# Kernel optimization log

Measured on AMD Instinct MI355X. Metric: run time of the kernel, lower is better.

The kernel has to match this reference:

```python
import jax, jax.numpy as jnp
import numpy as np

D_MODEL = 1024
N_HEADS = 16
HEAD_DIM = D_MODEL // N_HEADS


def setup_inputs() -> dict:
    key = jax.random.key(0)
    k_x, k_w1, k_b1, k_w2, k_b2 = jax.random.split(key, 5)
    B, S = 4, 2048
    x = jax.random.normal(k_x, (B, S, D_MODEL), dtype=jnp.float32)
    # torch Linear init ~ U(-1/sqrt(fan_in), 1/sqrt(fan_in))
    lim = 1.0 / np.sqrt(D_MODEL)
    qkv_w = jax.random.uniform(k_w1, (D_MODEL, 3 * D_MODEL), jnp.float32, -lim, lim)
    qkv_b = jax.random.uniform(k_b1, (3 * D_MODEL,), jnp.float32, -lim, lim)
    out_w = jax.random.uniform(k_w2, (D_MODEL, D_MODEL), jnp.float32, -lim, lim)
    out_b = jax.random.uniform(k_b2, (D_MODEL,), jnp.float32, -lim, lim)
    return {"x": x, "qkv_w": qkv_w, "qkv_b": qkv_b, "out_w": out_w, "out_b": out_b}


def reference(x, qkv_w, qkv_b, out_w, out_b):
    B, S, D = x.shape
    scale = HEAD_DIM ** -0.5
    qkv = x @ qkv_w + qkv_b  # [B,S,3D]
    q, k, v = jnp.split(qkv, 3, axis=-1)
    def to_heads(t):
        return t.reshape(B, S, N_HEADS, HEAD_DIM).transpose(0, 2, 1, 3)  # [B,H,S,Dh]
    q, k, v = to_heads(q), to_heads(k), to_heads(v)
    scores = jnp.einsum('bhqd,bhkd->bhqk', q, k) * scale  # [B,H,S,S]
    causal = jnp.tril(jnp.ones((S, S), dtype=bool))
    scores = jnp.where(causal, scores, -jnp.inf)
    weights = jax.nn.softmax(scores, axis=-1)  # dropout is identity in eval
    out = jnp.einsum('bhqk,bhkd->bhqd', weights, v)  # [B,H,S,Dh]
    out = out.transpose(0, 2, 1, 3).reshape(B, S, D)
    return out @ out_w + out_b
```

## Files before the change

kernel.cpp:

```cpp
#include <hip/hip_runtime.h>

typedef __bf16 bf16x8 __attribute__((ext_vector_type(8)));
typedef float f32x4 __attribute__((ext_vector_type(4)));
typedef unsigned short u16;

#define D_MODEL 1024
#define SEQ     2048
#define BATCH   4
#define NH      16
#define DH      64

#define QSCALE 0.18033688011f

#define SWZ(b) ((b) ^ ((((b) >> 8) & 3) << 5) ^ ((((b) >> 7) & 1) << 4))

static __device__ __forceinline__ u16 f2bf(float f) {
    union { float f; unsigned u; } v; v.f = f;
    unsigned r = v.u + 0x7FFF + ((v.u >> 16) & 1);
    return (u16)(r >> 16);
}
static __device__ __forceinline__ void storeC(u16* C, size_t off, float v) { C[off] = f2bf(v); }
static __device__ __forceinline__ void storeC(float* C, size_t off, float v) { C[off] = v; }

static __device__ __forceinline__ void async_ld16(u16* lds, const u16* g) {
    __builtin_amdgcn_global_load_lds(
        (const __attribute__((address_space(1))) unsigned int*)g,
        (__attribute__((address_space(3))) unsigned int*)lds, 16, 0, 0);
}

__global__ __launch_bounds__(256) void prepass(
    const float* __restrict__ x,     u16* __restrict__ xb,
    const float* __restrict__ qkv_w, u16* __restrict__ Wqkv_t,
    const float* __restrict__ out_w, u16* __restrict__ Wout_t) {
    __shared__ float tile[32][33];
    int bid = blockIdx.x, tid = threadIdx.x;

    if (bid < 4096) {
        size_t i = ((size_t)bid * 256 + tid) * 8;
        float4 a = *(const float4*)(x + i);
        float4 b = *(const float4*)(x + i + 4);
        u16 t[8] = {f2bf(a.x), f2bf(a.y), f2bf(a.z), f2bf(a.w),
                    f2bf(b.x), f2bf(b.y), f2bf(b.z), f2bf(b.w)};
        *(uint4*)(xb + i) = *(uint4*)t;
        return;
    }

    const float* in; u16* out; int n0, k0, N;
    if (bid < 7168) {
        int bb = bid - 4096;
        n0 = (bb % 96) * 32; k0 = (bb / 96) * 32;
        in = qkv_w; out = Wqkv_t; N = 3 * D_MODEL;
    } else {
        int bb = bid - 7168;
        n0 = (bb & 31) * 32; k0 = (bb >> 5) * 32;
        in = out_w; out = Wout_t; N = D_MODEL;
    }
    int tx = tid & 31, ty = tid >> 5;
    for (int i = ty; i < 32; i += 8)
        tile[i][tx] = in[(size_t)(k0 + i) * N + n0 + tx];
    __syncthreads();
    for (int i = ty; i < 32; i += 8)
        out[(size_t)(n0 + i) * D_MODEL + k0 + tx] = f2bf(tile[tx][i]);
}

template <typename CT>
__global__ __launch_bounds__(256) void gemm_bt(
    const u16* __restrict__ A, int lda,
    const u16* __restrict__ Bt, int ldb,
    const float* __restrict__ bias,
    CT* __restrict__ C, int ldc, int K) {
    __shared__ u16 As[2][128 * 64];
    __shared__ u16 Bs[2][128 * 64];
    int m0 = blockIdx.x * 128, n0 = blockIdx.y * 128;
    int tid = threadIdx.x;
    int w = tid >> 6, lane = tid & 63, l15 = lane & 15, g = lane >> 4;
    int wm = (w & 1) * 64, wn = (w >> 1) * 64;
    int srow = w * 8 + (lane >> 3);
    int sk8  = lane & 7;

    auto stage = [&](int buf, int kt) {
        #pragma unroll
        for (int p = 0; p < 4; ++p) {
            int row = p * 32 + srow;
            int k8 = sk8 ^ (row & 7);
            async_ld16(&As[buf][p * 2048 + w * 512],
                       A + (size_t)(m0 + row) * lda + kt + k8 * 8);
            async_ld16(&Bs[buf][p * 2048 + w * 512],
                       Bt + (size_t)(n0 + row) * ldb + kt + k8 * 8);
        }
    };

    f32x4 acc[4][4] = {};

    stage(0, 0);
    __syncthreads();
    for (int kt = 0; kt < K; kt += 64) {
        int cur = (kt >> 6) & 1;
        if (kt + 64 < K) stage(cur ^ 1, kt + 64);
        #pragma unroll
        for (int kk = 0; kk < 2; ++kk) {
            bf16x8 af[4], bf_[4];
            int s8 = ((kk << 2) | g) ^ (l15 & 7);
            #pragma unroll
            for (int i = 0; i < 4; ++i) {
                af[i]  = *(const bf16x8*)&As[cur][(wm + i * 16 + l15) * 64 + s8 * 8];
                bf_[i] = *(const bf16x8*)&Bs[cur][(wn + i * 16 + l15) * 64 + s8 * 8];
            }
            #pragma unroll
            for (int i = 0; i < 4; ++i)
                #pragma unroll
                for (int j = 0; j < 4; ++j)
                    acc[i][j] = __builtin_amdgcn_mfma_f32_16x16x32_bf16(
                        af[i], bf_[j], acc[i][j], 0, 0, 0);
        }
        __syncthreads();
    }
    #pragma unroll
    for (int j = 0; j < 4; ++j) {
        int n = n0 + wn + j * 16 + l15;
        float bv = bias[n];
        #pragma unroll
        for (int i = 0; i < 4; ++i) {
            int mbase = m0 + wm + i * 16 + g * 4;
            #pragma unroll
            for (int r = 0; r < 4; ++r)
                storeC(C, (size_t)(mbase + r) * ldc + n, acc[i][j][r] + bv);
        }
    }
}

__global__ __launch_bounds__(256) void gemm_qkv(
    const u16* __restrict__ A,
    const u16* __restrict__ Bt,
    const float* __restrict__ bias,
    u16* __restrict__ Qd, u16* __restrict__ pkK, u16* __restrict__ pkV) {
    __shared__ u16 As[2][128 * 64];
    __shared__ u16 Bs[2][128 * 64];
    const int K = D_MODEL;
    int m0 = blockIdx.x * 128, n0 = blockIdx.y * 128;
    int tid = threadIdx.x;
    int w = tid >> 6, lane = tid & 63, l15 = lane & 15, g = lane >> 4;
    int wm = (w & 1) * 64, wn = (w >> 1) * 64;
    int srow = w * 8 + (lane >> 3);
    int sk8  = lane & 7;

    auto stage = [&](int buf, int kt) {
        #pragma unroll
        for (int p = 0; p < 4; ++p) {
            int row = p * 32 + srow;
            int k8 = sk8 ^ (row & 7);
            async_ld16(&As[buf][p * 2048 + w * 512],
                       A + (size_t)(m0 + row) * K + kt + k8 * 8);
            async_ld16(&Bs[buf][p * 2048 + w * 512],
                       Bt + (size_t)(n0 + row) * K + kt + k8 * 8);
        }
    };

    f32x4 acc[4][4] = {};

    stage(0, 0);
    __syncthreads();
    for (int kt = 0; kt < K; kt += 64) {
        int cur = (kt >> 6) & 1;
        if (kt + 64 < K) stage(cur ^ 1, kt + 64);
        #pragma unroll
        for (int kk = 0; kk < 2; ++kk) {
            bf16x8 af[4], bf_[4];
            int s8 = ((kk << 2) | g) ^ (l15 & 7);
            #pragma unroll
            for (int i = 0; i < 4; ++i) {
                af[i]  = *(const bf16x8*)&As[cur][(wm + i * 16 + l15) * 64 + s8 * 8];
                bf_[i] = *(const bf16x8*)&Bs[cur][(wn + i * 16 + l15) * 64 + s8 * 8];
            }
            #pragma unroll
            for (int i = 0; i < 4; ++i)
                #pragma unroll
                for (int j = 0; j < 4; ++j)
                    acc[i][j] = __builtin_amdgcn_mfma_f32_16x16x32_bf16(
                        af[i], bf_[j], acc[i][j], 0, 0, 0);
        }
        __syncthreads();
    }

    int region = n0 >> 10;
    if (region == 0) {
        #pragma unroll
        for (int j = 0; j < 4; ++j) {
            int n = n0 + wn + j * 16 + l15;
            float bv = bias[n];
            int hd = n & 1023;
            #pragma unroll
            for (int i = 0; i < 4; ++i) {
                #pragma unroll
                for (int r = 0; r < 4; ++r) {
                    int m = m0 + wm + i * 16 + g * 4 + r;
                    Qd[(size_t)m * 1024 + hd] =
                        f2bf((acc[i][j][r] + bv) * QSCALE);
                }
            }
        }
        return;
    }

    char* lds = (char*)As;
    int h0 = (n0 & 1023) >> 6;
    int t0 = (m0 & 2047) >> 6;
    int bb = m0 >> 11;

    if (region == 1) {
        #pragma unroll
        for (int j = 0; j < 4; ++j) {
            int dn = wn + j * 16 + l15;
            float bv = bias[n0 + dn];
            int hp = dn >> 6, d = dn & 63;
            int kk = d >> 5, gk = (d >> 3) & 3, jk = d & 7;
            #pragma unroll
            for (int i = 0; i < 4; ++i) {
                #pragma unroll
                for (int r = 0; r < 4; ++r) {
                    int mm = wm + i * 16 + g * 4 + r;
                    int tp = mm >> 6, kap = mm & 63;
                    int nb = kap >> 4, lk = kap & 15;
                    int o = (((nb * 2 + kk) * 64 + gk * 16 + lk) * 8 + jk) * 2;
                    *(u16*)(lds + (hp * 2 + tp) * 8192 + SWZ(o)) =
                        f2bf(acc[i][j][r] + bv);
                }
            }
        }
    } else {
        #pragma unroll
        for (int j = 0; j < 4; ++j) {
            int dn = wn + j * 16 + l15;
            float bv = bias[n0 + dn];
            int hp = dn >> 6, d = dn & 63;
            int nb = d >> 4, lv = d & 15;
            #pragma unroll
            for (int i = 0; i < 4; ++i) {
                int mmb = wm + i * 16 + g * 4;
                int tp = mmb >> 6, kapb = mmb & 63;
                int kk = kapb >> 5, gv = (kapb >> 3) & 3, jvb = kapb & 7;
                union { u16 q[4]; unsigned long long ll; } p4;
                #pragma unroll
                for (int r = 0; r < 4; ++r)
                    p4.q[r] = f2bf(acc[i][j][r] + bv);
                int o = (((nb * 2 + kk) * 64 + gv * 16 + lv) * 8 + jvb) * 2;
                *(unsigned long long*)(lds + (hp * 2 + tp) * 8192 + SWZ(o)) =
                    p4.ll;
            }
        }
    }
    __syncthreads();
    u16* pk = (region == 1) ? pkK : pkV;
    #pragma unroll
    for (int c = 0; c < 4; ++c) {
        int hp = c >> 1, tp = c & 1;
        u16* dst = pk + ((size_t)((bb * 16 + h0 + hp) * 32) + t0 + tp) * 4096;
        int o0 = tid * 32, o1 = tid * 32 + 16;
        uint4 v0 = *(uint4*)(lds + c * 8192 + SWZ(o0));
        uint4 v1 = *(uint4*)(lds + c * 8192 + SWZ(o1));
        *(uint4*)&dst[tid * 16]     = v0;
        *(uint4*)&dst[tid * 16 + 8] = v1;
    }
}

__global__ __launch_bounds__(256) void attn_flash(
    u16* __restrict__ Qd, const u16* __restrict__ pkK,
    const u16* __restrict__ pkV) {
    __shared__ __align__(16) char smemraw[18432 + 256];
    u16 (*Pt)[32][72] = (u16(*)[32][72])smemraw;
    float* Om = (float*)smemraw;
    float* Lm = (float*)(smemraw + 18432);

    int bh = blockIdx.x, b = bh >> 4, h = bh & 15;
    int tid = threadIdx.x;
    int w = tid >> 6, lane = tid & 63, l15 = lane & 15, g = lane >> 4;
    int wq = w >> 1, wk = w & 1;

    const u16* Kb = pkK + (size_t)bh * 32 * 4096;
    const u16* Vb = pkV + (size_t)bh * 32 * 4096;
    u16* Qbase = Qd + (size_t)b * SEQ * 1024 + h * DH;

    int qts[2] = {31 - (int)blockIdx.y, (int)blockIdx.y};

    #pragma unroll
    for (int qi = 0; qi < 2; ++qi) {
        int qt = qts[qi];
        int q0 = qt * 64;

        bf16x8 qfrag[2][2];
        #pragma unroll
        for (int st = 0; st < 2; ++st) {
            const u16* qp = Qbase + (size_t)(q0 + wq * 32 + st * 16 + l15) * 1024 + g * 8;
            qfrag[st][0] = *(const bf16x8*)qp;
            qfrag[st][1] = *(const bf16x8*)(qp + 32);
        }

        f32x4 o[2][4] = {};
        float lsum[2][4] = {};

        auto ktile = [&](int t, bool diag) {
            const u16* kt = Kb + t * 4096;
            const u16* vt = Vb + t * 4096;
            bf16x8 kf[4][2], vf[4][2];
            #pragma unroll
            for (int nb = 0; nb < 4; ++nb) {
                #pragma unroll
                for (int kk = 0; kk < 2; ++kk) {
                    kf[nb][kk] = *(const bf16x8*)(kt + ((nb * 2 + kk) * 64 + lane) * 8);
                    vf[nb][kk] = *(const bf16x8*)(vt + ((nb * 2 + kk) * 64 + lane) * 8);
                }
            }
            int k0 = t * 64;

            #pragma unroll
            for (int st = 0; st < 2; ++st) {
                f32x4 s[4] = {};
                #pragma unroll
                for (int nb = 0; nb < 4; ++nb)
                    #pragma unroll
                    for (int kk = 0; kk < 2; ++kk)
                        s[nb] = __builtin_amdgcn_mfma_f32_16x16x32_bf16(
                            qfrag[st][kk], kf[nb][kk], s[nb], 0, 0, 0);

                #pragma unroll
                for (int r = 0; r < 4; ++r) {
                    int qg = q0 + wq * 32 + st * 16 + g * 4 + r;
                    #pragma unroll
                    for (int nb = 0; nb < 4; ++nb) {
                        float p = __builtin_amdgcn_exp2f(s[nb][r]);
                        if (diag && (k0 + nb * 16 + l15) > qg) p = 0.f;
                        lsum[st][r] += p;
                        Pt[w][st * 16 + g * 4 + r][nb * 16 + l15] =
                            (u16)(__float_as_uint(p) >> 16);
                    }
                }

                #pragma unroll
                for (int kk = 0; kk < 2; ++kk) {
                    bf16x8 aP = *(const bf16x8*)&Pt[w][st * 16 + l15][kk * 32 + g * 8];
                    #pragma unroll
                    for (int nb = 0; nb < 4; ++nb)
                        o[st][nb] = __builtin_amdgcn_mfma_f32_16x16x32_bf16(
                            aP, vf[nb][kk], o[st][nb], 0, 0, 0);
                }
            }
        };

        for (int t = wk; t < qt; t += 2) ktile(t, false);
        if ((qt & 1) == wk) ktile(qt, true);

        #pragma unroll
        for (int msk = 1; msk < 16; msk <<= 1)
            #pragma unroll
            for (int st = 0; st < 2; ++st)
                #pragma unroll
                for (int r = 0; r < 4; ++r)
                    lsum[st][r] += __shfl_xor(lsum[st][r], msk, 64);

        __syncthreads();
        if (wk == 0) {
            #pragma unroll
            for (int st = 0; st < 2; ++st)
                #pragma unroll
                for (int r = 0; r < 4; ++r) {
                    int qrow = wq * 32 + st * 16 + g * 4 + r;
                    if (l15 == 0) Lm[qrow] = lsum[st][r];
                    #pragma unroll
                    for (int nb = 0; nb < 4; ++nb)
                        Om[qrow * 65 + nb * 16 + l15] = o[st][nb][r];
                }
        }
        __syncthreads();
        if (wk == 1) {
            #pragma unroll
            for (int st = 0; st < 2; ++st)
                #pragma unroll
                for (int r = 0; r < 4; ++r) {
                    int qrow = wq * 32 + st * 16 + g * 4 + r;
                    float inv = 1.f / (lsum[st][r] + Lm[qrow]);
                    u16* op = Qbase + (size_t)(q0 + qrow) * 1024;
                    #pragma unroll
                    for (int nb = 0; nb < 4; ++nb) {
                        float val = (o[st][nb][r] + Om[qrow * 65 + nb * 16 + l15]) * inv;
                        op[nb * 16 + l15] = f2bf(val);
                    }
                }
        }
        __syncthreads();
    }
}

extern "C" void kernel_launch(void* const* d_in, const int* in_sizes, int n_in,
                              void* d_out, int out_size, void* d_ws, size_t ws_size,
                              hipStream_t stream) {
    const float* x     = (const float*)d_in[0];
    const float* qkv_w = (const float*)d_in[1];
    const float* qkv_b = (const float*)d_in[2];
    const float* out_w = (const float*)d_in[3];
    const float* out_b = (const float*)d_in[4];
    float* out = (float*)d_out;

    const int M = BATCH * SEQ;
    u16* Qd     = (u16*)d_ws;
    u16* pkK    = Qd  + (size_t)M * D_MODEL;
    u16* pkV    = pkK + (size_t)64 * 32 * 4096;
    u16* xb     = pkV + (size_t)64 * 32 * 4096;
    u16* Wqkv_t = xb  + (size_t)M * D_MODEL;
    u16* Wout_t = Wqkv_t + (size_t)3 * D_MODEL * D_MODEL;

    prepass<<<dim3(8192), 256, 0, stream>>>(x, xb, qkv_w, Wqkv_t, out_w, Wout_t);

    gemm_qkv<<<dim3(M / 128, 3 * D_MODEL / 128), 256, 0, stream>>>(
        xb, Wqkv_t, qkv_b, Qd, pkK, pkV);

    attn_flash<<<dim3(BATCH * NH, SEQ / 64 / 2), 256, 0, stream>>>(Qd, pkK, pkV);

    gemm_bt<float><<<dim3(M / 128, D_MODEL / 128), 256, 0, stream>>>(
        Qd, D_MODEL, Wout_t, D_MODEL, out_b, out, D_MODEL, D_MODEL);
}
```

Before: 241.9 us.

## Restructure attention to one query tile per 2-wave block without KV split

The attention kernel now launches one 128-thread block per 64-row query tile, longest tiles first. Before, each 256-thread block handled a paired long and short tile, with two wave pairs splitting the key tiles and merging partial outputs through shared memory. Removing the intra-block KV split drops the LDS merge and the three barriers, and doubles the number of blocks. In exchange each wave walks the full causal key range serially, so per-block latency for long tiles grows, and the causal load balance now relies on the hardware scheduler rather than explicit tile pairing.

After: 228.5 us. 1.06x faster.

```diff
diff --git a/kernel.cpp b/kernel.cpp
--- a/kernel.cpp
+++ b/kernel.cpp
@@ -263,131 +263,103 @@
     }
 }
 
-__global__ __launch_bounds__(256) void attn_flash(
+__global__ __launch_bounds__(128) void attn_flash(
     u16* __restrict__ Qd, const u16* __restrict__ pkK,
     const u16* __restrict__ pkV) {
-    __shared__ __align__(16) char smemraw[18432 + 256];
-    u16 (*Pt)[32][72] = (u16(*)[32][72])smemraw;
-    float* Om = (float*)smemraw;
-    float* Lm = (float*)(smemraw + 18432);
+    __shared__ __align__(16) u16 Pt[2][32][72];
 
     int bh = blockIdx.x, b = bh >> 4, h = bh & 15;
     int tid = threadIdx.x;
     int w = tid >> 6, lane = tid & 63, l15 = lane & 15, g = lane >> 4;
-    int wq = w >> 1, wk = w & 1;
 
     const u16* Kb = pkK + (size_t)bh * 32 * 4096;
     const u16* Vb = pkV + (size_t)bh * 32 * 4096;
     u16* Qbase = Qd + (size_t)b * SEQ * 1024 + h * DH;
 
-    int qts[2] = {31 - (int)blockIdx.y, (int)blockIdx.y};
-
-    #pragma unroll
-    for (int qi = 0; qi < 2; ++qi) {
-        int qt = qts[qi];
-        int q0 = qt * 64;
-
-        bf16x8 qfrag[2][2];
+    int qt = 31 - (int)blockIdx.y;
+    int q0 = qt * 64;
+
+    bf16x8 qfrag[2][2];
+    #pragma unroll
+    for (int st = 0; st < 2; ++st) {
+        const u16* qp = Qbase + (size_t)(q0 + w * 32 + st * 16 + l15) * 1024 + g * 8;
+        qfrag[st][0] = *(const bf16x8*)qp;
+        qfrag[st][1] = *(const bf16x8*)(qp + 32);
+    }
+
+    f32x4 o[2][4] = {};
+    float lsum[2][4] = {};
+
+    auto ktile = [&](int t, bool diag) {
+        const u16* kt = Kb + t * 4096;
+        const u16* vt = Vb + t * 4096;
+        bf16x8 kf[4][2], vf[4][2];
+        #pragma unroll
+        for (int nb = 0; nb < 4; ++nb) {
+            #pragma unroll
+            for (int kk = 0; kk < 2; ++kk) {
+                kf[nb][kk] = *(const bf16x8*)(kt + ((nb * 2 + kk) * 64 + lane) * 8);
+                vf[nb][kk] = *(const bf16x8*)(vt + ((nb * 2 + kk) * 64 + lane) * 8);
+            }
+        }
+        int k0 = t * 64;
+
         #pragma unroll
         for (int st = 0; st < 2; ++st) {
-            const u16* qp = Qbase + (size_t)(q0 + wq * 32 + st * 16 + l15) * 1024 + g * 8;
-            qfrag[st][0] = *(const bf16x8*)qp;
-            qfrag[st][1] = *(const bf16x8*)(qp + 32);
-        }
-
-        f32x4 o[2][4] = {};
-        float lsum[2][4] = {};
-
-        auto ktile = [&](int t, bool diag) {
-            const u16* kt = Kb + t * 4096;
-            const u16* vt = Vb + t * 4096;
-            bf16x8 kf[4][2], vf[4][2];
-            #pragma unroll
-            for (int nb = 0; nb < 4; ++nb) {
-                #pragma unroll
-                for (int kk = 0; kk < 2; ++kk) {
-                    kf[nb][kk] = *(const bf16x8*)(kt + ((nb * 2 + kk) * 64 + lane) * 8);
-                    vf[nb][kk] = *(const bf16x8*)(vt + ((nb * 2 + kk) * 64 + lane) * 8);
+            f32x4 s[4] = {};
+            #pragma unroll
+            for (int nb = 0; nb < 4; ++nb)
+                #pragma unroll
+                for (int kk = 0; kk < 2; ++kk)
+                    s[nb] = __builtin_amdgcn_mfma_f32_16x16x32_bf16(
+                        qfrag[st][kk], kf[nb][kk], s[nb], 0, 0, 0);
+
+            #pragma unroll
+            for (int r = 0; r < 4; ++r) {
+                int qg = q0 + w * 32 + st * 16 + g * 4 + r;
+                #pragma unroll
+                for (int nb = 0; nb < 4; ++nb) {
+                    float p = __builtin_amdgcn_exp2f(s[nb][r]);
+                    if (diag && (k0 + nb * 16 + l15) > qg) p = 0.f;
+                    lsum[st][r] += p;
+                    Pt[w][st * 16 + g * 4 + r][nb * 16 + l15] =
+                        (u16)(__float_as_uint(p) >> 16);
                 }
             }
-            int k0 = t * 64;
-
-            #pragma unroll
-            for (int st = 0; st < 2; ++st) {
-                f32x4 s[4] = {};
+
+            #pragma unroll
+            for (int kk = 0; kk < 2; ++kk) {
+                bf16x8 aP = *(const bf16x8*)&Pt[w][st * 16 + l15][kk * 32 + g * 8];
                 #pragma unroll
                 for (int nb = 0; nb < 4; ++nb)
-                    #pragma unroll
-                    for (int kk = 0; kk < 2; ++kk)
-                        s[nb] = __builtin_amdgcn_mfma_f32_16x16x32_bf16(
-                            qfrag[st][kk], kf[nb][kk], s[nb], 0, 0, 0);
-
-                #pragma unroll
-                for (int r = 0; r < 4; ++r) {
-                    int qg = q0 + wq * 32 + st * 16 + g * 4 + r;
-                    #pragma unroll
-                    for (int nb = 0; nb < 4; ++nb) {
-                        float p = __builtin_amdgcn_exp2f(s[nb][r]);
-                        if (diag && (k0 + nb * 16 + l15) > qg) p = 0.f;
-                        lsum[st][r] += p;
-                        Pt[w][st * 16 + g * 4 + r][nb * 16 + l15] =
-                            (u16)(__float_as_uint(p) >> 16);
-                    }
-                }
-
-                #pragma unroll
-                for (int kk = 0; kk < 2; ++kk) {
-                    bf16x8 aP = *(const bf16x8*)&Pt[w][st * 16 + l15][kk * 32 + g * 8];
-                    #pragma unroll
-                    for (int nb = 0; nb < 4; ++nb)
-                        o[st][nb] = __builtin_amdgcn_mfma_f32_16x16x32_bf16(
-                            aP, vf[nb][kk], o[st][nb], 0, 0, 0);
-                }
-            }
-        };
-
-        for (int t = wk; t < qt; t += 2) ktile(t, false);
-        if ((qt & 1) == wk) ktile(qt, true);
-
-        #pragma unroll
-        for (int msk = 1; msk < 16; msk <<= 1)
-            #pragma unroll
-            for (int st = 0; st < 2; ++st)
-                #pragma unroll
-                for (int r = 0; r < 4; ++r)
-                    lsum[st][r] += __shfl_xor(lsum[st][r], msk, 64);
-
-        __syncthreads();
-        if (wk == 0) {
-            #pragma unroll
-            for (int st = 0; st < 2; ++st)
-                #pragma unroll
-                for (int r = 0; r < 4; ++r) {
-                    int qrow = wq * 32 + st * 16 + g * 4 + r;
-                    if (l15 == 0) Lm[qrow] = lsum[st][r];
-                    #pragma unroll
-                    for (int nb = 0; nb < 4; ++nb)
-                        Om[qrow * 65 + nb * 16 + l15] = o[st][nb][r];
-                }
-        }
-        __syncthreads();
-        if (wk == 1) {
-            #pragma unroll
-            for (int st = 0; st < 2; ++st)
-                #pragma unroll
-                for (int r = 0; r < 4; ++r) {
-                    int qrow = wq * 32 + st * 16 + g * 4 + r;
-                    float inv = 1.f / (lsum[st][r] + Lm[qrow]);
-                    u16* op = Qbase + (size_t)(q0 + qrow) * 1024;
-                    #pragma unroll
-                    for (int nb = 0; nb < 4; ++nb) {
-                        float val = (o[st][nb][r] + Om[qrow * 65 + nb * 16 + l15]) * inv;
-                        op[nb * 16 + l15] = f2bf(val);
-                    }
-                }
-        }
-        __syncthreads();
-    }
+                    o[st][nb] = __builtin_amdgcn_mfma_f32_16x16x32_bf16(
+                        aP, vf[nb][kk], o[st][nb], 0, 0, 0);
+            }
+        }
+    };
+
+    for (int t = 0; t < qt; ++t) ktile(t, false);
+    ktile(qt, true);
+
+    #pragma unroll
+    for (int msk = 1; msk < 16; msk <<= 1)
+        #pragma unroll
+        for (int st = 0; st < 2; ++st)
+            #pragma unroll
+            for (int r = 0; r < 4; ++r)
+                lsum[st][r] += __shfl_xor(lsum[st][r], msk, 64);
+
+    #pragma unroll
+    for (int st = 0; st < 2; ++st)
+        #pragma unroll
+        for (int r = 0; r < 4; ++r) {
+            int qrow = w * 32 + st * 16 + g * 4 + r;
+            float inv = 1.f / lsum[st][r];
+            u16* op = Qbase + (size_t)(q0 + qrow) * 1024;
+            #pragma unroll
+            for (int nb = 0; nb < 4; ++nb)
+                op[nb * 16 + l15] = f2bf(o[st][nb][r] * inv);
+        }
 }
 
 extern "C" void kernel_launch(void* const* d_in, const int* in_sizes, int n_in,
@@ -413,7 +385,7 @@
     gemm_qkv<<<dim3(M / 128, 3 * D_MODEL / 128), 256, 0, stream>>>(
         xb, Wqkv_t, qkv_b, Qd, pkK, pkV);
 
-    attn_flash<<<dim3(BATCH * NH, SEQ / 64 / 2), 256, 0, stream>>>(Qd, pkK, pkV);
+    attn_flash<<<dim3(BATCH * NH, SEQ / 64), 128, 0, stream>>>(Qd, pkK, pkV);
 
     gemm_bt<float><<<dim3(M / 128, D_MODEL / 128), 256, 0, stream>>>(
         Qd, D_MODEL, Wout_t, D_MODEL, out_b, out, D_MODEL, D_MODEL);
```
